# Optimization experiments

Measured on AMD Instinct MI355X. Metric: run time of the kernel, lower is better.

Reference implementation:

```python
import jax, jax.numpy as jnp
import numpy as np

N, B, K, D_IN, D_OUT = 100000, 20000, 32, 256, 256
NEG = -1000000.0


def setup_inputs() -> dict:
    key = jax.random.key(0)
    ks = jax.random.split(key, 6)
    return {
        "word_vec": jax.random.normal(ks[0], (N, D_IN), dtype=jnp.float32),
        "W1": jax.random.normal(ks[1], (D_OUT, D_IN), dtype=jnp.float32) * (1.0 / np.sqrt(D_IN)),
        "W_aux": jax.random.normal(ks[2], (1, 4), dtype=jnp.float32),
        "aux": jax.random.normal(ks[3], (B, K, 4), dtype=jnp.float32),
        "src_idx": jnp.arange(B, dtype=jnp.int32),
        "neighs_idx": jax.random.randint(ks[4], (B, K), 0, N, dtype=jnp.int32),
        "src_mask": jax.random.randint(ks[5], (B, K), 0, 2, dtype=jnp.int32),
    }


def reference(word_vec, W1, W_aux, aux, src_idx, neighs_idx, src_mask):
    supports = word_vec  # dropout disabled -> identity
    q = supports[src_idx]                    # [B, D]
    k = supports[neighs_idx]                 # [B, K, D]
    scores = jnp.einsum("bd,bkd->bk", q, k) * 5.0              # [B, K]
    scores_aux = jax.nn.sigmoid(jnp.einsum("bkf,of->bko", aux, W_aux)).reshape(B, K)
    mask = src_mask == 1
    p1 = jax.nn.softmax(jnp.where(mask, scores, NEG), axis=-1)       # [B, K]
    p2 = jax.nn.softmax(jnp.where(mask, scores_aux, NEG), axis=-1)   # [B, K]
    proj = jax.nn.leaky_relu(word_vec @ W1.T, negative_slope=0.2)    # [N, D_OUT]
    agg = jnp.einsum("bk,bkd->bd", (p1 + p2) * 0.5, proj[neighs_idx])  # [B, D_OUT]
    return proj.at[src_idx].set(agg)
```

## Files before the change

### kernel.cpp

```cpp
#include <hip/hip_runtime.h>
#include <cstdint>

#define N_NODES 100000
#define BQ      20000
#define KN      32
#define NEGV    -1000000.0f

typedef float    f32x4 __attribute__((ext_vector_type(4)));
typedef _Float16 h16x4 __attribute__((ext_vector_type(4)));
typedef _Float16 h16x8 __attribute__((ext_vector_type(8)));

__device__ __forceinline__ int imin(int a, int b) { return a < b ? a : b; }

#define GLOAD_LDS16(g, l)                                                      \
    __builtin_amdgcn_global_load_lds(                                          \
        (const __attribute__((address_space(1))) unsigned int*)(g),            \
        (__attribute__((address_space(3))) unsigned int*)(l), 16, 0, 0)

__global__ __launch_bounds__(256) void prep_f16(const float* __restrict__ wv,
                                                _Float16* __restrict__ ws16) {
    const int stride = gridDim.x * blockDim.x;
    const int total = N_NODES * 32;
    for (int i = blockIdx.x * blockDim.x + threadIdx.x; i < total; i += stride) {
        const size_t e = (size_t)i * 8;
        const size_t n = e >> 8, c = e & 255;
        f32x4 a = __builtin_nontemporal_load((const f32x4*)&wv[e]);
        f32x4 b = __builtin_nontemporal_load((const f32x4*)&wv[e + 4]);
        h16x8 h = {(_Float16)a[0], (_Float16)a[1], (_Float16)a[2], (_Float16)a[3],
                   (_Float16)b[0], (_Float16)b[1], (_Float16)b[2], (_Float16)b[3]};
        *(h16x8*)&ws16[n * 512 + c] = h;
    }
}

__global__ __launch_bounds__(256, 2) void proj_gemm(const _Float16* __restrict__ ws16,
                                                    const float* __restrict__ W,
                                                    float* __restrict__ out,
                                                    _Float16* __restrict__ pjdst) {
    __shared__ _Float16 As[2][64 * 64];

    const int m0 = blockIdx.x * 64;
    const int t = threadIdx.x;
    const int lane = t & 63;
    const int w = t >> 6;
    const int wn = w * 64;

    const int chs = ((lane & 7) ^ (lane >> 3)) * 16;
    {
#pragma unroll
        for (int i = 0; i < 2; ++i) {
            const int r0 = w * 16 + i * 8;
            const int grow = imin(m0 + r0 + (lane >> 3), N_NODES - 1);
            const char* g = (const char*)ws16 + (size_t)grow * 1024 + chs;
            GLOAD_LDS16(g, (char*)&As[0][0] + r0 * 128);
        }
    }

    h16x8 bq[4][8];
#pragma unroll
    for (int ni = 0; ni < 4; ++ni) {
#pragma unroll
        for (int ks = 0; ks < 8; ++ks) {
            const int nrow = wn + ni * 16 + (lane & 15);
            const int kb = ks * 32 + (lane >> 4) * 8;
            f32x4 v0 = *(const f32x4*)&W[(size_t)nrow * 256 + kb];
            f32x4 v1 = *(const f32x4*)&W[(size_t)nrow * 256 + kb + 4];
            bq[ni][ks] = h16x8{(_Float16)v0[0], (_Float16)v0[1], (_Float16)v0[2],
                               (_Float16)v0[3], (_Float16)v1[0], (_Float16)v1[1],
                               (_Float16)v1[2], (_Float16)v1[3]};
        }
    }

    f32x4 acc[4][4];
#pragma unroll
    for (int i = 0; i < 4; ++i)
#pragma unroll
        for (int j = 0; j < 4; ++j) acc[i][j] = f32x4{0.f, 0.f, 0.f, 0.f};

    asm volatile("s_waitcnt vmcnt(0)" ::: "memory");
    __syncthreads();

#pragma unroll
    for (int kk = 0; kk < 4; ++kk) {
        const int cur = kk & 1;
        if (kk < 3) {
#pragma unroll
            for (int i = 0; i < 2; ++i) {
                const int r0 = w * 16 + i * 8;
                const int grow = imin(m0 + r0 + (lane >> 3), N_NODES - 1);
                const char* g =
                    (const char*)ws16 + (size_t)grow * 1024 + (kk + 1) * 128 + chs;
                GLOAD_LDS16(g, (char*)&As[cur ^ 1][0] + r0 * 128);
            }
        }
#pragma unroll
        for (int ksl = 0; ksl < 2; ++ksl) {
            const int colb = ksl * 64 + ((lane >> 4) * 16);
            h16x8 af[4];
#pragma unroll
            for (int mi = 0; mi < 4; ++mi) {
                const int row = mi * 16 + (lane & 15);
                const int byte = row * 128 + (colb ^ ((row & 7) << 4));
                af[mi] = *(const h16x8*)((const char*)&As[cur][0] + byte);
            }
#pragma unroll
            for (int mi = 0; mi < 4; ++mi)
#pragma unroll
                for (int ni = 0; ni < 4; ++ni)
                    acc[mi][ni] = __builtin_amdgcn_mfma_f32_16x16x32_f16(
                        af[mi], bq[ni][kk * 2 + ksl], acc[mi][ni], 0, 0, 0);
        }
        asm volatile("s_waitcnt vmcnt(0)" ::: "memory");
        __syncthreads();
    }

    const int cr = (lane >> 4) * 4;
    const int cc = lane & 15;
#pragma unroll
    for (int mi = 0; mi < 4; ++mi) {
#pragma unroll
        for (int r = 0; r < 4; ++r) {
            const int grow = m0 + mi * 16 + cr + r;
            if (grow < N_NODES) {
#pragma unroll
                for (int ni = 0; ni < 4; ++ni) {
                    float v = acc[mi][ni][r];
                    v = v > 0.f ? v : 0.2f * v;
                    const int col = wn + ni * 16 + cc;
                    __builtin_nontemporal_store(v, &out[(size_t)grow * 256 + col]);
                    pjdst[(size_t)grow * 512 + 256 + col] = (_Float16)v;
                }
            }
        }
    }
}

__global__ __launch_bounds__(256) void att_agg16(const _Float16* __restrict__ ws16,
                                                 const float* __restrict__ Waux,
                                                 const float* __restrict__ aux,
                                                 const int* __restrict__ src_idx,
                                                 const int* __restrict__ nidx,
                                                 const int* __restrict__ smask,
                                                 float* __restrict__ out) {
    __shared__ int   nsh[32];
    __shared__ int   msh[32];
    __shared__ float sc[32];
    __shared__ float sa[32];
    __shared__ float wsh[32];
    __shared__ float part[4][64][4];

    const int b = blockIdx.x;
    const int t = threadIdx.x;
    const int lane = t & 63;
    const int w = t >> 6;
    const int src = src_idx[b];

    if (t < 32) {
        nsh[t] = nidx[b * KN + t];
        msh[t] = smask[b * KN + t];
        f32x4 a4 = __builtin_nontemporal_load((const f32x4*)&aux[((size_t)b * KN + t) * 4]);
        const float x = a4[0] * Waux[0] + a4[1] * Waux[1] + a4[2] * Waux[2] + a4[3] * Waux[3];
        sa[t] = 1.f / (1.f + expf(-x));
    }
    const h16x4 qh = *(const h16x4*)&ws16[(size_t)src * 512 + lane * 4];
    const float q0 = (float)qh[0], q1 = (float)qh[1], q2 = (float)qh[2], q3 = (float)qh[3];
    __syncthreads();

    int nk[8];
#pragma unroll
    for (int i = 0; i < 8; ++i) nk[i] = nsh[w * 8 + i];

    h16x4 k4[8], v4[8];
#pragma unroll
    for (int i = 0; i < 8; ++i)
        k4[i] = *(const h16x4*)&ws16[(size_t)nk[i] * 512 + lane * 4];
#pragma unroll
    for (int i = 0; i < 8; ++i)
        v4[i] = *(const h16x4*)&ws16[(size_t)nk[i] * 512 + 256 + lane * 4];

#pragma unroll
    for (int i = 0; i < 8; ++i) {
        float p = q0 * (float)k4[i][0] + q1 * (float)k4[i][1] + q2 * (float)k4[i][2] +
                  q3 * (float)k4[i][3];
#pragma unroll
        for (int o = 32; o > 0; o >>= 1) p += __shfl_xor(p, o);
        if (lane == 0) sc[w * 8 + i] = 5.f * p;
    }
    __syncthreads();

    if (t < 32) {
        const bool mk = (msh[t] == 1);
        const float s1 = mk ? sc[t] : NEGV;
        const float s2 = mk ? sa[t] : NEGV;
        float m1 = s1, m2 = s2;
#pragma unroll
        for (int o = 16; o > 0; o >>= 1) {
            m1 = fmaxf(m1, __shfl_xor(m1, o));
            m2 = fmaxf(m2, __shfl_xor(m2, o));
        }
        const float e1 = expf(s1 - m1), e2 = expf(s2 - m2);
        float z1 = e1, z2 = e2;
#pragma unroll
        for (int o = 16; o > 0; o >>= 1) {
            z1 += __shfl_xor(z1, o);
            z2 += __shfl_xor(z2, o);
        }
        wsh[t] = 0.5f * (e1 / z1 + e2 / z2);
    }
    __syncthreads();

    f32x4 pacc = f32x4{0.f, 0.f, 0.f, 0.f};
#pragma unroll
    for (int i = 0; i < 8; ++i) {
        const float wk = wsh[w * 8 + i];
#pragma unroll
        for (int j = 0; j < 4; ++j) pacc[j] += wk * (float)v4[i][j];
    }
    *(f32x4*)&part[w][lane][0] = pacc;
    __syncthreads();

    if (w == 0) {
        f32x4 s0 = *(const f32x4*)&part[0][lane][0];
        f32x4 s1 = *(const f32x4*)&part[1][lane][0];
        f32x4 s2 = *(const f32x4*)&part[2][lane][0];
        f32x4 s3 = *(const f32x4*)&part[3][lane][0];
        f32x4 s;
#pragma unroll
        for (int j = 0; j < 4; ++j) s[j] = (s0[j] + s1[j]) + (s2[j] + s3[j]);
        __builtin_nontemporal_store(s, (f32x4*)&out[(size_t)src * 256 + lane * 4]);
    }
}

extern "C" void kernel_launch(void* const* d_in, const int* in_sizes, int n_in,
                              void* d_out, int out_size, void* d_ws, size_t ws_size,
                              hipStream_t stream) {
    const float* wv   = (const float*)d_in[0];
    const float* W1   = (const float*)d_in[1];
    const float* Waux = (const float*)d_in[2];
    const float* aux  = (const float*)d_in[3];
    const int*   src  = (const int*)d_in[4];
    const int*   nidx = (const int*)d_in[5];
    const int*   smk  = (const int*)d_in[6];
    float* out = (float*)d_out;
    _Float16* ws16 = (_Float16*)d_ws;

    prep_f16<<<dim3(4096), dim3(256), 0, stream>>>(wv, ws16);
    proj_gemm<<<dim3((N_NODES + 63) / 64), dim3(256), 0, stream>>>(ws16, W1, out, ws16);
    att_agg16<<<dim3(BQ), dim3(256), 0, stream>>>(ws16, Waux, aux, src, nidx, smk, out);
}
```

Baseline: 361.0 us.

## Fuse fp16 conversion into projection GEMM, loading fp32 operands directly

Removes the separate prep kernel that converted word_vec to fp16 in the workspace. The GEMM now reads fp32 rows of word_vec and W straight from global memory into registers, converts them, and writes the fp16 copy of word_vec needed by the attention kernel as it goes. This drops the LDS double buffering and async global-to-LDS loads, and W is reloaded for each k-step instead of being held in registers. The goal is to avoid one kernel launch and a full extra pass over word_vec, at the cost of less latency hiding and redundant per-wave loads of the A tile, since every wave loads all 64 rows.

```diff
diff --git a/kernel.cpp b/kernel.cpp
--- a/kernel.cpp
+++ b/kernel.cpp
@@ -12,63 +12,17 @@
 
 __device__ __forceinline__ int imin(int a, int b) { return a < b ? a : b; }
 
-#define GLOAD_LDS16(g, l)                                                      \
-    __builtin_amdgcn_global_load_lds(                                          \
-        (const __attribute__((address_space(1))) unsigned int*)(g),            \
-        (__attribute__((address_space(3))) unsigned int*)(l), 16, 0, 0)
-
-__global__ __launch_bounds__(256) void prep_f16(const float* __restrict__ wv,
-                                                _Float16* __restrict__ ws16) {
-    const int stride = gridDim.x * blockDim.x;
-    const int total = N_NODES * 32;
-    for (int i = blockIdx.x * blockDim.x + threadIdx.x; i < total; i += stride) {
-        const size_t e = (size_t)i * 8;
-        const size_t n = e >> 8, c = e & 255;
-        f32x4 a = __builtin_nontemporal_load((const f32x4*)&wv[e]);
-        f32x4 b = __builtin_nontemporal_load((const f32x4*)&wv[e + 4]);
-        h16x8 h = {(_Float16)a[0], (_Float16)a[1], (_Float16)a[2], (_Float16)a[3],
-                   (_Float16)b[0], (_Float16)b[1], (_Float16)b[2], (_Float16)b[3]};
-        *(h16x8*)&ws16[n * 512 + c] = h;
-    }
-}
-
-__global__ __launch_bounds__(256, 2) void proj_gemm(const _Float16* __restrict__ ws16,
-                                                    const float* __restrict__ W,
-                                                    float* __restrict__ out,
-                                                    _Float16* __restrict__ pjdst) {
-    __shared__ _Float16 As[2][64 * 64];
-
+__global__ __launch_bounds__(256) void proj_fused(const float* __restrict__ wv,
+                                                  const float* __restrict__ W,
+                                                  float* __restrict__ out,
+                                                  _Float16* __restrict__ ws16) {
     const int m0 = blockIdx.x * 64;
     const int t = threadIdx.x;
     const int lane = t & 63;
     const int w = t >> 6;
     const int wn = w * 64;
-
-    const int chs = ((lane & 7) ^ (lane >> 3)) * 16;
-    {
-#pragma unroll
-        for (int i = 0; i < 2; ++i) {
-            const int r0 = w * 16 + i * 8;
-            const int grow = imin(m0 + r0 + (lane >> 3), N_NODES - 1);
-            const char* g = (const char*)ws16 + (size_t)grow * 1024 + chs;
-            GLOAD_LDS16(g, (char*)&As[0][0] + r0 * 128);
-        }
-    }
-
-    h16x8 bq[4][8];
-#pragma unroll
-    for (int ni = 0; ni < 4; ++ni) {
-#pragma unroll
-        for (int ks = 0; ks < 8; ++ks) {
-            const int nrow = wn + ni * 16 + (lane & 15);
-            const int kb = ks * 32 + (lane >> 4) * 8;
-            f32x4 v0 = *(const f32x4*)&W[(size_t)nrow * 256 + kb];
-            f32x4 v1 = *(const f32x4*)&W[(size_t)nrow * 256 + kb + 4];
-            bq[ni][ks] = h16x8{(_Float16)v0[0], (_Float16)v0[1], (_Float16)v0[2],
-                               (_Float16)v0[3], (_Float16)v1[0], (_Float16)v1[1],
-                               (_Float16)v1[2], (_Float16)v1[3]};
-        }
-    }
+    const int rg = lane & 15;
+    const int g = lane >> 4;
 
     f32x4 acc[4][4];
 #pragma unroll
@@ -76,45 +30,46 @@
 #pragma unroll
         for (int j = 0; j < 4; ++j) acc[i][j] = f32x4{0.f, 0.f, 0.f, 0.f};
 
-    asm volatile("s_waitcnt vmcnt(0)" ::: "memory");
-    __syncthreads();
-
-#pragma unroll
-    for (int kk = 0; kk < 4; ++kk) {
-        const int cur = kk & 1;
-        if (kk < 3) {
-#pragma unroll
-            for (int i = 0; i < 2; ++i) {
-                const int r0 = w * 16 + i * 8;
-                const int grow = imin(m0 + r0 + (lane >> 3), N_NODES - 1);
-                const char* g =
-                    (const char*)ws16 + (size_t)grow * 1024 + (kk + 1) * 128 + chs;
-                GLOAD_LDS16(g, (char*)&As[cur ^ 1][0] + r0 * 128);
+#pragma unroll
+    for (int ks = 0; ks < 8; ++ks) {
+        const int kc = ks * 32 + g * 8;
+
+        h16x8 bq[4];
+#pragma unroll
+        for (int ni = 0; ni < 4; ++ni) {
+            const float* p = &W[(size_t)(wn + ni * 16 + rg) * 256 + kc];
+            f32x4 b0 = *(const f32x4*)p;
+            f32x4 b1 = *(const f32x4*)(p + 4);
+            bq[ni] = h16x8{(_Float16)b0[0], (_Float16)b0[1], (_Float16)b0[2],
+                           (_Float16)b0[3], (_Float16)b1[0], (_Float16)b1[1],
+                           (_Float16)b1[2], (_Float16)b1[3]};
+        }
+
+        h16x8 af[4];
+#pragma unroll
+        for (int mi = 0; mi < 4; ++mi) {
+            const int r = imin(m0 + mi * 16 + rg, N_NODES - 1);
+            const float* p = &wv[(size_t)r * 256 + kc];
+            f32x4 a0 = *(const f32x4*)p;
+            f32x4 a1 = *(const f32x4*)(p + 4);
+            af[mi] = h16x8{(_Float16)a0[0], (_Float16)a0[1], (_Float16)a0[2],
+                           (_Float16)a0[3], (_Float16)a1[0], (_Float16)a1[1],
+                           (_Float16)a1[2], (_Float16)a1[3]};
+            if (mi == w) {
+                const int rw = m0 + mi * 16 + rg;
+                if (rw < N_NODES) *(h16x8*)&ws16[(size_t)rw * 512 + kc] = af[mi];
             }
         }
-#pragma unroll
-        for (int ksl = 0; ksl < 2; ++ksl) {
-            const int colb = ksl * 64 + ((lane >> 4) * 16);
-            h16x8 af[4];
-#pragma unroll
-            for (int mi = 0; mi < 4; ++mi) {
-                const int row = mi * 16 + (lane & 15);
-                const int byte = row * 128 + (colb ^ ((row & 7) << 4));
-                af[mi] = *(const h16x8*)((const char*)&As[cur][0] + byte);
-            }
-#pragma unroll
-            for (int mi = 0; mi < 4; ++mi)
-#pragma unroll
-                for (int ni = 0; ni < 4; ++ni)
-                    acc[mi][ni] = __builtin_amdgcn_mfma_f32_16x16x32_f16(
-                        af[mi], bq[ni][kk * 2 + ksl], acc[mi][ni], 0, 0, 0);
-        }
-        asm volatile("s_waitcnt vmcnt(0)" ::: "memory");
-        __syncthreads();
-    }
-
-    const int cr = (lane >> 4) * 4;
-    const int cc = lane & 15;
+
+#pragma unroll
+        for (int mi = 0; mi < 4; ++mi)
+#pragma unroll
+            for (int ni = 0; ni < 4; ++ni)
+                acc[mi][ni] = __builtin_amdgcn_mfma_f32_16x16x32_f16(af[mi], bq[ni],
+                                                                     acc[mi][ni], 0, 0, 0);
+    }
+
+    const int cr = g * 4;
 #pragma unroll
     for (int mi = 0; mi < 4; ++mi) {
 #pragma unroll
@@ -125,9 +80,9 @@
                 for (int ni = 0; ni < 4; ++ni) {
                     float v = acc[mi][ni][r];
                     v = v > 0.f ? v : 0.2f * v;
-                    const int col = wn + ni * 16 + cc;
+                    const int col = wn + ni * 16 + rg;
                     __builtin_nontemporal_store(v, &out[(size_t)grow * 256 + col]);
-                    pjdst[(size_t)grow * 512 + 256 + col] = (_Float16)v;
+                    ws16[(size_t)grow * 512 + 256 + col] = (_Float16)v;
                 }
             }
         }
@@ -243,7 +198,6 @@
     float* out = (float*)d_out;
     _Float16* ws16 = (_Float16*)d_ws;
 
-    prep_f16<<<dim3(4096), dim3(256), 0, stream>>>(wv, ws16);
-    proj_gemm<<<dim3((N_NODES + 63) / 64), dim3(256), 0, stream>>>(ws16, W1, out, ws16);
+    proj_fused<<<dim3((N_NODES + 63) / 64), dim3(256), 0, stream>>>(wv, W1, out, ws16);
     att_agg16<<<dim3(BQ), dim3(256), 0, stream>>>(ws16, Waux, aux, src, nidx, smk, out);
 }
```

After: 392.2 us. 1.09x slower.
